# Kernel tuning notes

Measured on AMD Instinct MI355X. Metric: run time of the kernel, lower is better.

The kernel has to match this reference:

```python
import jax, jax.numpy as jnp
import numpy as np
from jax import lax

# Model hyperparameters (match init_kwargs)
DIM = 512
N_HEADS = 8
HEAD_DIM = DIM // N_HEADS
N_LAYERS = 4
N_LEVELS = 3          # len(chunk_sizes); CMS forward = stack of MLPs per level
HIDDEN = 4 * DIM
VOCAB = 50257
MAX_SEQ = 2048
B, S = 1, 2048
LN_EPS = 1e-5


def layer_norm(x, w, b):
    m = x.mean(-1, keepdims=True)
    v = ((x - m) ** 2).mean(-1, keepdims=True)
    return (x - m) * lax.rsqrt(v + LN_EPS) * w + b


def linear_attention(x, wq, wk, wv, wo):
    """LinearAttentionWithMemory: fast-weight recurrence M += k v^T, ksum += k,
    y_t = (M_t q_t) / (ksum_t . q_t + 1e-6). x: (B,S,DIM). Weights stored (in,out)."""
    Bn, Sn, D = x.shape
    fmap = lambda z: jax.nn.elu(z) + 1.0  # elu(x)+1 feature map
    # (B,S,D) -> (S,B,H,d) for scan over time
    def proj(w):
        return fmap(x @ w).reshape(Bn, Sn, N_HEADS, HEAD_DIM).transpose(1, 0, 2, 3)
    q = proj(wq)
    k = proj(wk)
    v = fmap(x @ wv).reshape(Bn, Sn, N_HEADS, HEAD_DIM).transpose(1, 0, 2, 3)
    # NOTE: original applies feature_map only to Q and K; V is raw projection
    v = (x @ wv).reshape(Bn, Sn, N_HEADS, HEAD_DIM).transpose(1, 0, 2, 3)

    def step(carry, inp):
        M, ksum = carry            # M: (B,H,d,d), ksum: (B,H,d)
        q_t, k_t, v_t = inp        # each (B,H,d)
        M = M + k_t[..., :, None] * v_t[..., None, :]
        ksum = ksum + k_t
        num = jnp.einsum('bhde,bhd->bhe', M, q_t)
        den = jnp.einsum('bhd,bhd->bh', ksum, q_t)[..., None] + 1e-6
        return (M, ksum), num / den

    carry0 = (jnp.zeros((Bn, N_HEADS, HEAD_DIM, HEAD_DIM), x.dtype),
              jnp.zeros((Bn, N_HEADS, HEAD_DIM), x.dtype))
    _, ys = lax.scan(step, carry0, (q, k, v))          # ys: (S,B,H,d)
    out = ys.transpose(1, 0, 2, 3).reshape(Bn, Sn, D)
    return out @ wo


def cms(x, w1, b1, w2, b2):
    """Continuum Memory System forward: sequential chain of per-level MLPs
    (chunk sizes only control parameter-update frequency during training).
    w1: (N_LEVELS, DIM, HIDDEN), w2: (N_LEVELS, HIDDEN, DIM)."""
    h = x
    for lvl in range(N_LEVELS):
        h = jax.nn.gelu(h @ w1[lvl] + b1[lvl]) @ w2[lvl] + b2[lvl]
    return h


def setup_inputs() -> dict:
    key = jax.random.key(0)
    ks = jax.random.split(key, 16)
    std = 0.02
    inp = {
        'tok_emb': jax.random.normal(ks[0], (VOCAB, DIM), jnp.float32) * std,
        'pos_emb': jax.random.normal(ks[1], (MAX_SEQ, DIM), jnp.float32) * std,
        'ln1_w': jnp.ones((N_LAYERS, DIM), jnp.float32),
        'ln1_b': jnp.zeros((N_LAYERS, DIM), jnp.float32),
        'wq': jax.random.normal(ks[2], (N_LAYERS, DIM, DIM), jnp.float32) * std,
        'wk': jax.random.normal(ks[3], (N_LAYERS, DIM, DIM), jnp.float32) * std,
        'wv': jax.random.normal(ks[4], (N_LAYERS, DIM, DIM), jnp.float32) * std,
        'wo': jax.random.normal(ks[5], (N_LAYERS, DIM, DIM), jnp.float32) * std,
        'ln2_w': jnp.ones((N_LAYERS, DIM), jnp.float32),
        'ln2_b': jnp.zeros((N_LAYERS, DIM), jnp.float32),
        'cms_w1': jax.random.normal(ks[6], (N_LAYERS, N_LEVELS, DIM, HIDDEN), jnp.float32) * std,
        'cms_b1': jnp.zeros((N_LAYERS, N_LEVELS, HIDDEN), jnp.float32),
        'cms_w2': jax.random.normal(ks[7], (N_LAYERS, N_LEVELS, HIDDEN, DIM), jnp.float32) * std,
        'cms_b2': jnp.zeros((N_LAYERS, N_LEVELS, DIM), jnp.float32),
        'lnf_w': jnp.ones((DIM,), jnp.float32),
        'lnf_b': jnp.zeros((DIM,), jnp.float32),
        'input_ids': jax.random.randint(ks[8], (B, S), 0, VOCAB, jnp.int32),
    }
    return inp


def reference(tok_emb, pos_emb, ln1_w, ln1_b, wq, wk, wv, wo,
              ln2_w, ln2_b, cms_w1, cms_b1, cms_w2, cms_b2,
              lnf_w, lnf_b, input_ids):
    seq_len = input_ids.shape[1]
    x = tok_emb[input_ids] + pos_emb[:seq_len][None, :, :]
    for l in range(N_LAYERS):
        x = x + linear_attention(layer_norm(x, ln1_w[l], ln1_b[l]),
                                 wq[l], wk[l], wv[l], wo[l])
        x = x + cms(layer_norm(x, ln2_w[l], ln2_b[l]),
                    cms_w1[l], cms_b1[l], cms_w2[l], cms_b2[l])
    x = layer_norm(x, lnf_w, lnf_b)
    logits = x @ tok_emb.T  # tied head weights
    return logits
```

## Files before the change

kernel.cpp:

```cpp
#include <hip/hip_runtime.h>

#define SQL 2048
#define DIM 512
#define NHEADS 8
#define HD 64
#define NLAYERS 4
#define NLEVELS 3
#define HID 2048
#define VOC 50257
#define CHUNK 64
#define NCHUNK 32
#define SD (SQL * DIM)
#define DD (DIM * DIM)

typedef __attribute__((ext_vector_type(8))) short bf16x8;
typedef __attribute__((ext_vector_type(4))) float f32x4;

__device__ __forceinline__ float gelu_f(float x) {
    float x3 = x * x * x;
    return 0.5f * x * (1.f + tanhf(0.7978845608028654f * (x + 0.044715f * x3)));
}
__device__ __forceinline__ float fmap_f(float x) {
    return x > 0.f ? x + 1.f : expf(x);
}
__device__ __forceinline__ unsigned short f2bf(float x) {
    unsigned int u = __float_as_uint(x);
    u = (u + 0x7fffu + ((u >> 16) & 1u)) >> 16;
    return (unsigned short)u;
}
__device__ __forceinline__ float bf2f(unsigned short h) {
    return __uint_as_float(((unsigned int)h) << 16);
}

__global__ __launch_bounds__(256) void embed_k(
    const float* __restrict__ tok, const float* __restrict__ pos,
    const int* __restrict__ ids, float* __restrict__ x)
{
    int idx = blockIdx.x * 256 + threadIdx.x;
    int t = idx >> 9;
    int d = idx & 511;
    x[idx] = tok[(size_t)ids[t] * DIM + d] + pos[idx];
}

__global__ __launch_bounds__(256) void ln_k(
    const float* __restrict__ in, unsigned short* __restrict__ oh,
    unsigned short* __restrict__ ol,
    const float* __restrict__ w, const float* __restrict__ b)
{
    int t = blockIdx.x, tid = threadIdx.x;
    float v0 = in[t * DIM + tid];
    float v1 = in[t * DIM + 256 + tid];
    float s = v0 + v1, sq = v0 * v0 + v1 * v1;
    #pragma unroll
    for (int off = 32; off > 0; off >>= 1) {
        s  += __shfl_down(s, off);
        sq += __shfl_down(sq, off);
    }
    __shared__ float ss[4], sqs[4];
    int wave = tid >> 6, lane = tid & 63;
    if (lane == 0) { ss[wave] = s; sqs[wave] = sq; }
    __syncthreads();
    float S  = ss[0] + ss[1] + ss[2] + ss[3];
    float SQ = sqs[0] + sqs[1] + sqs[2] + sqs[3];
    float m   = S * (1.f / DIM);
    float var = SQ * (1.f / DIM) - m * m;
    float rs  = rsqrtf(var + 1e-5f);
    float y0 = (v0 - m) * rs * w[tid]       + b[tid];
    float y1 = (v1 - m) * rs * w[256 + tid] + b[256 + tid];
    unsigned short h0 = f2bf(y0), h1 = f2bf(y1);
    oh[t * DIM + tid]       = h0;
    ol[t * DIM + tid]       = f2bf(y0 - bf2f(h0));
    oh[t * DIM + 256 + tid] = h1;
    ol[t * DIM + 256 + tid] = f2bf(y1 - bf2f(h1));
}

__global__ __launch_bounds__(256) void conv_rh_k(
    const float* __restrict__ in, unsigned short* __restrict__ oh, long long n4)
{
    long long i = (long long)blockIdx.x * 256 + threadIdx.x;
    if (i >= n4) return;
    float4 v = ((const float4*)in)[i];
    ushort4 hh;
    hh.x = f2bf(v.x); hh.y = f2bf(v.y); hh.z = f2bf(v.z); hh.w = f2bf(v.w);
    ((ushort4*)oh)[i] = hh;
}

__global__ __launch_bounds__(256) void conv_t_k(
    const float* __restrict__ in, unsigned short* __restrict__ oh,
    unsigned short* __restrict__ ol, int K, int N,
    size_t srcZ, size_t dstZ)
{
    in += (size_t)blockIdx.z * srcZ;
    oh += (size_t)blockIdx.z * dstZ;
    ol += (size_t)blockIdx.z * dstZ;
    __shared__ float T[32][33];
    const int n0 = blockIdx.x * 32, k0 = blockIdx.y * 32;
    const int tr = threadIdx.x >> 3, tc = threadIdx.x & 7;
    float4 v = *(const float4*)(in + (size_t)(k0 + tr) * N + n0 + tc * 4);
    T[tr][tc * 4 + 0] = v.x;
    T[tr][tc * 4 + 1] = v.y;
    T[tr][tc * 4 + 2] = v.z;
    T[tr][tc * 4 + 3] = v.w;
    __syncthreads();
    float o0 = T[tc * 4 + 0][tr];
    float o1 = T[tc * 4 + 1][tr];
    float o2 = T[tc * 4 + 2][tr];
    float o3 = T[tc * 4 + 3][tr];
    unsigned short h0 = f2bf(o0), h1 = f2bf(o1), h2 = f2bf(o2), h3 = f2bf(o3);
    ushort4 hh; hh.x = h0; hh.y = h1; hh.z = h2; hh.w = h3;
    ushort4 ll;
    ll.x = f2bf(o0 - bf2f(h0));
    ll.y = f2bf(o1 - bf2f(h1));
    ll.z = f2bf(o2 - bf2f(h2));
    ll.w = f2bf(o3 - bf2f(h3));
    size_t off = (size_t)(n0 + tr) * K + k0 + tc * 4;
    *(ushort4*)(oh + off) = hh;
    *(ushort4*)(ol + off) = ll;
}

template<int ACT, bool RES, bool PLANES, bool NG, bool X3, bool MSWAP, int BN>
__global__ __launch_bounds__(256) void gemm_t(
    const unsigned short* __restrict__ Ah, const unsigned short* __restrict__ Al,
    const unsigned short* __restrict__ Bh, const unsigned short* __restrict__ Bl,
    const float* __restrict__ bias, const float* __restrict__ Rsrc,
    float* __restrict__ C, unsigned short* __restrict__ Oh,
    unsigned short* __restrict__ Ol,
    int M, int N, int K, int fthr)
{
    constexpr int NW = BN / 2;
    constexpr int NF = NW / 16;
    __shared__ unsigned short sAh[4096], sAl[4096];
    __shared__ unsigned short sBh[BN * 32];
    __shared__ unsigned short sBl[X3 ? BN * 32 : 64];

    const int tid  = threadIdx.x;
    const int w    = tid >> 6, lane = tid & 63;
    const int r    = lane & 15, kq = lane >> 4;
    const int wr   = w >> 1, wc = w & 1;
    const int m0   = (MSWAP ? blockIdx.x : blockIdx.y) * 128;
    const int n0   = (MSWAP ? blockIdx.y : blockIdx.x) * BN;

    const int srow = tid >> 2;
    const int sch  = tid & 3;
    const int ar0 = m0 + srow, ar1 = ar0 + 64;
    int br0 = n0 + srow;
    if (NG) br0 = br0 < N ? br0 : N - 1;
    const unsigned short* pAh0 = Ah + (size_t)ar0 * K + sch * 8;
    const unsigned short* pAh1 = Ah + (size_t)ar1 * K + sch * 8;
    const unsigned short* pAl0 = Al + (size_t)ar0 * K + sch * 8;
    const unsigned short* pAl1 = Al + (size_t)ar1 * K + sch * 8;
    const unsigned short* pBh0 = Bh + (size_t)br0 * K + sch * 8;
    const unsigned short* pBl0 = X3 ? Bl + (size_t)br0 * K + sch * 8 : nullptr;
    const unsigned short* pBh1 = nullptr;
    const unsigned short* pBl1 = nullptr;
    if constexpr (BN == 128) {
        int br1 = n0 + 64 + srow;
        if (NG) br1 = br1 < N ? br1 : N - 1;
        pBh1 = Bh + (size_t)br1 * K + sch * 8;
        if constexpr (X3) pBl1 = Bl + (size_t)br1 * K + sch * 8;
    }

    bf16x8 rAh0 = *(const bf16x8*)pAh0, rAh1 = *(const bf16x8*)pAh1;
    bf16x8 rAl0 = *(const bf16x8*)pAl0, rAl1 = *(const bf16x8*)pAl1;
    bf16x8 rBh0 = *(const bf16x8*)pBh0;
    bf16x8 rBh1{}, rBl0{}, rBl1{};
    if constexpr (X3) rBl0 = *(const bf16x8*)pBl0;
    if constexpr (BN == 128) {
        rBh1 = *(const bf16x8*)pBh1;
        if constexpr (X3) rBl1 = *(const bf16x8*)pBl1;
    }

    f32x4 acc[4][NF] = {};
    const int sw = tid * 8;

    for (int ks = 0; ks < K; ks += 32) {
        __syncthreads();
        *(bf16x8*)&sAh[sw] = rAh0;  *(bf16x8*)&sAh[sw + 2048] = rAh1;
        *(bf16x8*)&sAl[sw] = rAl0;  *(bf16x8*)&sAl[sw + 2048] = rAl1;
        *(bf16x8*)&sBh[sw] = rBh0;
        if constexpr (BN == 128) *(bf16x8*)&sBh[sw + 2048] = rBh1;
        if constexpr (X3) {
            *(bf16x8*)&sBl[sw] = rBl0;
            if constexpr (BN == 128) *(bf16x8*)&sBl[sw + 2048] = rBl1;
        }
        __syncthreads();

        if (ks + 32 < K) {
            pAh0 += 32; pAh1 += 32; pAl0 += 32; pAl1 += 32;
            pBh0 += 32;
            rAh0 = *(const bf16x8*)pAh0; rAh1 = *(const bf16x8*)pAh1;
            rAl0 = *(const bf16x8*)pAl0; rAl1 = *(const bf16x8*)pAl1;
            rBh0 = *(const bf16x8*)pBh0;
            if constexpr (X3) { pBl0 += 32; rBl0 = *(const bf16x8*)pBl0; }
            if constexpr (BN == 128) {
                pBh1 += 32; rBh1 = *(const bf16x8*)pBh1;
                if constexpr (X3) { pBl1 += 32; rBl1 = *(const bf16x8*)pBl1; }
            }
        }

        bf16x8 a_h[4], a_l[4];
        #pragma unroll
        for (int mi = 0; mi < 4; ++mi) {
            const int off = (wr * 64 + mi * 16 + r) * 32 + kq * 8;
            a_h[mi] = *(const bf16x8*)&sAh[off];
            a_l[mi] = *(const bf16x8*)&sAl[off];
        }
        #pragma unroll
        for (int ni = 0; ni < NF; ++ni) {
            const int off = (wc * NW + ni * 16 + r) * 32 + kq * 8;
            const bf16x8 b_h = *(const bf16x8*)&sBh[off];
            #pragma unroll
            for (int mi = 0; mi < 4; ++mi) {
                acc[mi][ni] = __builtin_amdgcn_mfma_f32_16x16x32_bf16(
                    a_h[mi], b_h, acc[mi][ni], 0, 0, 0);
                acc[mi][ni] = __builtin_amdgcn_mfma_f32_16x16x32_bf16(
                    a_l[mi], b_h, acc[mi][ni], 0, 0, 0);
            }
            if constexpr (X3) {
                const bf16x8 b_l = *(const bf16x8*)&sBl[off];
                #pragma unroll
                for (int mi = 0; mi < 4; ++mi)
                    acc[mi][ni] = __builtin_amdgcn_mfma_f32_16x16x32_bf16(
                        a_h[mi], b_l, acc[mi][ni], 0, 0, 0);
            }
        }
    }

    #pragma unroll
    for (int mi = 0; mi < 4; ++mi)
        #pragma unroll
        for (int ni = 0; ni < NF; ++ni) {
            const int nn = n0 + wc * NW + ni * 16 + r;
            if (NG && nn >= N) continue;
            #pragma unroll
            for (int g = 0; g < 4; ++g) {
                const int mm = m0 + wr * 64 + mi * 16 + kq * 4 + g;
                float v = acc[mi][ni][g];
                if (bias) v += bias[nn];
                if (ACT == 2) v = gelu_f(v);
                if (ACT == 3) v = (nn < fthr) ? fmap_f(v) : v;
                const size_t o = (size_t)mm * N + nn;
                if (PLANES) {
                    unsigned short h = f2bf(v);
                    Oh[o] = h;
                    Ol[o] = f2bf(v - bf2f(h));
                } else {
                    if (RES) v += Rsrc[o];
                    C[o] = v;
                }
            }
        }
}

template<int ACT, bool RES, bool PLANES>
__global__ __launch_bounds__(256) void gemm_ks(
    const unsigned short* __restrict__ Ah, const unsigned short* __restrict__ Al,
    const unsigned short* __restrict__ Bh, const unsigned short* __restrict__ Bl,
    const float* __restrict__ bias, const float* __restrict__ Rsrc,
    float* __restrict__ C, unsigned short* __restrict__ Oh,
    unsigned short* __restrict__ Ol,
    int M, int N, int K, int fthr)
{
    const int tid  = threadIdx.x;
    const int w    = tid >> 6;
    const int lane = tid & 63;
    const int r  = lane & 15;
    const int kq = lane >> 4;
    const int m0 = blockIdx.y * 64, n0 = blockIdx.x * 64;
    const int Kw = K >> 2;

    f32x4 acc[4][4] = {};

    size_t aoff[4], boff[4];
    #pragma unroll
    for (int i = 0; i < 4; ++i) {
        aoff[i] = (size_t)(m0 + i * 16 + r) * K + w * Kw + kq * 8;
        boff[i] = (size_t)(n0 + i * 16 + r) * K + w * Kw + kq * 8;
    }

    for (int k0 = 0; k0 < Kw; k0 += 32) {
        bf16x8 ah[4], al4[4], bh[4], bl4[4];
        #pragma unroll
        for (int i = 0; i < 4; ++i) {
            ah[i]  = *(const bf16x8*)(Ah + aoff[i] + k0);
            al4[i] = *(const bf16x8*)(Al + aoff[i] + k0);
            bh[i]  = *(const bf16x8*)(Bh + boff[i] + k0);
            bl4[i] = *(const bf16x8*)(Bl + boff[i] + k0);
        }
        #pragma unroll
        for (int mi = 0; mi < 4; ++mi)
            #pragma unroll
            for (int ni = 0; ni < 4; ++ni) {
                acc[mi][ni] = __builtin_amdgcn_mfma_f32_16x16x32_bf16(
                    ah[mi], bh[ni], acc[mi][ni], 0, 0, 0);
                acc[mi][ni] = __builtin_amdgcn_mfma_f32_16x16x32_bf16(
                    ah[mi], bl4[ni], acc[mi][ni], 0, 0, 0);
                acc[mi][ni] = __builtin_amdgcn_mfma_f32_16x16x32_bf16(
                    al4[mi], bh[ni], acc[mi][ni], 0, 0, 0);
            }
    }

    __shared__ f32x4 red[4][64][8];

    #pragma unroll
    for (int R = 0; R < 2; ++R) {
        if (R) __syncthreads();
        #pragma unroll
        for (int mh = 0; mh < 2; ++mh) {
            const int mi = R * 2 + mh;
            const int q2 = mh * 4 + kq;
            #pragma unroll
            for (int ni = 0; ni < 4; ++ni) {
                const int cc = ni * 16 + r;
                red[w][cc][q2 ^ (cc & 7)] = acc[mi][ni];
            }
        }
        __syncthreads();
        const int col = lane;
        #pragma unroll
        for (int g = 0; g < 2; ++g) {
            const int q2 = w * 2 + g;
            const int swz = q2 ^ (col & 7);
            f32x4 s = red[0][col][swz];
            s += red[1][col][swz];
            s += red[2][col][swz];
            s += red[3][col][swz];
            const int gn = n0 + col;
            float bv = bias ? bias[gn] : 0.f;
            #pragma unroll
            for (int e = 0; e < 4; ++e) {
                const int gm = m0 + R * 32 + q2 * 4 + e;
                float v = s[e] + bv;
                if (ACT == 2) v = gelu_f(v);
                if (ACT == 3) v = (gn < fthr) ? fmap_f(v) : v;
                const size_t o = (size_t)gm * N + gn;
                if (PLANES) {
                    unsigned short h = f2bf(v);
                    Oh[o] = h;
                    Ol[o] = f2bf(v - bf2f(h));
                } else {
                    if (RES) v += Rsrc[o];
                    C[o] = v;
                }
            }
        }
    }
}

__global__ __launch_bounds__(256) void attn_p1(
    const float* __restrict__ kbuf, const float* __restrict__ vbuf,
    float* __restrict__ Mc, float* __restrict__ ksum, int rs)
{
    const int h = blockIdx.x >> 5, c = blockIdx.x & 31;
    const int tid = threadIdx.x;
    const int tx = tid & 15, ty = tid >> 4;
    __shared__ float Ks[CHUNK][HD + 1];
    __shared__ float Vs[CHUNK][HD + 1];
    #pragma unroll
    for (int i = 0; i < 16; ++i) {
        int idx = tid + i * 256;
        int t = idx >> 6, d = idx & 63;
        size_t g = (size_t)(c * CHUNK + t) * rs + h * HD + d;
        Ks[t][d] = kbuf[g];
        Vs[t][d] = vbuf[g];
    }
    __syncthreads();

    float acc[4][4] = {};
    for (int t = 0; t < CHUNK; ++t) {
        float ka[4], vb[4];
        #pragma unroll
        for (int i = 0; i < 4; ++i) ka[i] = Ks[t][ty * 4 + i];
        #pragma unroll
        for (int j = 0; j < 4; ++j) vb[j] = Vs[t][tx * 4 + j];
        #pragma unroll
        for (int i = 0; i < 4; ++i)
            #pragma unroll
            for (int j = 0; j < 4; ++j)
                acc[i][j] += ka[i] * vb[j];
    }
    const size_t base = (size_t)(h * NCHUNK + c) * HD * HD;
    #pragma unroll
    for (int i = 0; i < 4; ++i)
        #pragma unroll
        for (int j = 0; j < 4; ++j)
            Mc[base + (size_t)(ty * 4 + i) * HD + tx * 4 + j] = acc[i][j];

    if (tid < HD) {
        float s = 0.f;
        for (int t = 0; t < CHUNK; ++t) s += Ks[t][tid];
        ksum[(size_t)(h * NCHUNK + c) * HD + tid] = s;
    }
}

__global__ __launch_bounds__(64) void attn_scan(
    float* __restrict__ Mc, float* __restrict__ ksum)
{
    const int b = blockIdx.x;
    const int h = b / 65, p = b % 65;
    const int tid = threadIdx.x;
    float v[NCHUNK];
    if (p < HD) {
        const size_t base = ((size_t)(h * NCHUNK) * HD + p) * HD + tid;
        #pragma unroll
        for (int c = 0; c < NCHUNK; ++c)
            v[c] = Mc[base + (size_t)c * HD * HD];
        float run = 0.f;
        #pragma unroll
        for (int c = 0; c < NCHUNK; ++c) {
            Mc[base + (size_t)c * HD * HD] = run;
            run += v[c];
        }
    } else {
        const size_t base = (size_t)(h * NCHUNK) * HD + tid;
        #pragma unroll
        for (int c = 0; c < NCHUNK; ++c)
            v[c] = ksum[base + (size_t)c * HD];
        float run = 0.f;
        #pragma unroll
        for (int c = 0; c < NCHUNK; ++c) {
            ksum[base + (size_t)c * HD] = run;
            run += v[c];
        }
    }
}

__global__ __launch_bounds__(256) void attn_p3(
    const float* __restrict__ qbuf, const float* __restrict__ kbuf,
    const float* __restrict__ vbuf, const float* __restrict__ Mc,
    const float* __restrict__ ksum,
    unsigned short* __restrict__ aoh, unsigned short* __restrict__ aol, int rs)
{
    const int h = blockIdx.x >> 5, c = blockIdx.x & 31;
    const int tid = threadIdx.x;
    const int tx = tid & 15, ty = tid >> 4;
    __shared__ float Qs[CHUNK][HD + 1];
    __shared__ float Ks[CHUNK][HD + 1];
    __shared__ float Vs[CHUNK][HD + 1];
    __shared__ float Ss[CHUNK][CHUNK + 1];
    __shared__ float Ms[HD][HD + 1];
    __shared__ float kp[HD], den[CHUNK];

    const size_t mbase = (size_t)(h * NCHUNK + c) * HD * HD;
    #pragma unroll
    for (int i = 0; i < 16; ++i) {
        int idx = tid + i * 256;
        int t = idx >> 6, d = idx & 63;
        size_t g = (size_t)(c * CHUNK + t) * rs + h * HD + d;
        Qs[t][d] = qbuf[g];
        Ks[t][d] = kbuf[g];
        Vs[t][d] = vbuf[g];
        Ms[t][d] = Mc[mbase + (size_t)t * HD + d];
    }
    if (tid < HD) kp[tid] = ksum[(size_t)(h * NCHUNK + c) * HD + tid];
    __syncthreads();

    {
        float acc[4][4] = {};
        for (int d = 0; d < HD; ++d) {
            float qa[4], kb[4];
            #pragma unroll
            for (int i = 0; i < 4; ++i) qa[i] = Qs[ty * 4 + i][d];
            #pragma unroll
            for (int j = 0; j < 4; ++j) kb[j] = Ks[tx * 4 + j][d];
            #pragma unroll
            for (int i = 0; i < 4; ++i)
                #pragma unroll
                for (int j = 0; j < 4; ++j)
                    acc[i][j] += qa[i] * kb[j];
        }
        #pragma unroll
        for (int i = 0; i < 4; ++i)
            #pragma unroll
            for (int j = 0; j < 4; ++j) {
                int t = ty * 4 + i, u = tx * 4 + j;
                Ss[t][u] = (u <= t) ? acc[i][j] : 0.f;
            }
    }
    __syncthreads();

    if (tid < CHUNK) {
        int t = tid;
        float s = 1e-6f;
        for (int d = 0; d < HD; ++d) s += Qs[t][d] * kp[d];
        for (int u = 0; u < CHUNK; ++u) s += Ss[t][u];
        den[t] = s;
    }
    __syncthreads();

    {
        float acc[4][4] = {};
        for (int d = 0; d < HD; ++d) {
            float qa[4], mb[4];
            #pragma unroll
            for (int i = 0; i < 4; ++i) qa[i] = Qs[ty * 4 + i][d];
            #pragma unroll
            for (int j = 0; j < 4; ++j) mb[j] = Ms[d][tx * 4 + j];
            #pragma unroll
            for (int i = 0; i < 4; ++i)
                #pragma unroll
                for (int j = 0; j < 4; ++j)
                    acc[i][j] += qa[i] * mb[j];
        }
        for (int u = 0; u < CHUNK; ++u) {
            float sa[4], vb[4];
            #pragma unroll
            for (int i = 0; i < 4; ++i) sa[i] = Ss[ty * 4 + i][u];
            #pragma unroll
            for (int j = 0; j < 4; ++j) vb[j] = Vs[u][tx * 4 + j];
            #pragma unroll
            for (int i = 0; i < 4; ++i)
                #pragma unroll
                for (int j = 0; j < 4; ++j)
                    acc[i][j] += sa[i] * vb[j];
        }
        #pragma unroll
        for (int i = 0; i < 4; ++i) {
            int t = ty * 4 + i;
            float inv = 1.f / den[t];
            #pragma unroll
            for (int j = 0; j < 4; ++j) {
                float vv = acc[i][j] * inv;
                unsigned short hh = f2bf(vv);
                size_t o = (size_t)(c * CHUNK + t) * DIM + h * HD + tx * 4 + j;
                aoh[o] = hh;
                aol[o] = f2bf(vv - bf2f(hh));
            }
        }
    }
}

extern "C" void kernel_launch(void* const* d_in, const int* in_sizes, int n_in,
                              void* d_out, int out_size, void* d_ws, size_t ws_size,
                              hipStream_t stream)
{
    const float* tok  = (const float*)d_in[0];
    const float* pos  = (const float*)d_in[1];
    const float* ln1w = (const float*)d_in[2];
    const float* ln1b = (const float*)d_in[3];
    const float* wq   = (const float*)d_in[4];
    const float* wk   = (const float*)d_in[5];
    const float* wv   = (const float*)d_in[6];
    const float* wo   = (const float*)d_in[7];
    const float* ln2w = (const float*)d_in[8];
    const float* ln2b = (const float*)d_in[9];
    const float* w1   = (const float*)d_in[10];
    const float* b1   = (const float*)d_in[11];
    const float* w2   = (const float*)d_in[12];
    const float* b2   = (const float*)d_in[13];
    const float* lnfw = (const float*)d_in[14];
    const float* lnfb = (const float*)d_in[15];
    const int*   ids  = (const int*)d_in[16];
    float* outp = (float*)d_out;

    typedef unsigned short us;
    char* p = (char*)d_ws;
    float* x   = (float*)p; p += (size_t)SD * 4;
    float* qkv = (float*)p; p += (size_t)SQL * 3 * DIM * 4;
    float* Mc  = (float*)p; p += (size_t)NHEADS * NCHUNK * HD * HD * 4;
    float* ksm = (float*)p; p += (size_t)NHEADS * NCHUNK * HD * 4;

    us* xnH = (us*)p; p += (size_t)SD * 2;
    us* xnL = (us*)p; p += (size_t)SD * 2;
    us* aoH = (us*)p; p += (size_t)SD * 2;
    us* aoL = (us*)p; p += (size_t)SD * 2;
    us* cinH = (us*)p; p += (size_t)SD * 2;
    us* cinL = (us*)p; p += (size_t)SD * 2;
    us* h1H = (us*)p; p += (size_t)SQL * HID * 2;
    us* h1L = (us*)p; p += (size_t)SQL * HID * 2;
    us* tokH = (us*)p; p += (size_t)VOC * DIM * 2;
    us* wqkvH = (us*)p; p += (size_t)NLAYERS * 3 * DD * 2;
    us* wqkvL = (us*)p; p += (size_t)NLAYERS * 3 * DD * 2;
    us* woH = (us*)p; p += (size_t)NLAYERS * DD * 2;
    us* woL = (us*)p; p += (size_t)NLAYERS * DD * 2;
    const size_t W1SZ = (size_t)NLAYERS * NLEVELS * DIM * HID;
    us* w1H = (us*)p; p += W1SZ * 2;
    us* w1L = (us*)p; p += W1SZ * 2;
    us* w2H = (us*)p; p += W1SZ * 2;
    us* w2L = (us*)p; p += W1SZ * 2;

    {
        long long n4 = (long long)VOC * DIM / 4;
        conv_rh_k<<<(unsigned)((n4 + 255) / 256), 256, 0, stream>>>(tok, tokH, n4);
        dim3 gt(DIM / 32, DIM / 32, NLAYERS);
        conv_t_k<<<gt, 256, 0, stream>>>(wq, wqkvH,          wqkvL,          DIM, DIM, DD, (size_t)3 * DD);
        conv_t_k<<<gt, 256, 0, stream>>>(wk, wqkvH + DD,     wqkvL + DD,     DIM, DIM, DD, (size_t)3 * DD);
        conv_t_k<<<gt, 256, 0, stream>>>(wv, wqkvH + 2 * DD, wqkvL + 2 * DD, DIM, DIM, DD, (size_t)3 * DD);
        conv_t_k<<<gt, 256, 0, stream>>>(wo, woH, woL, DIM, DIM, DD, DD);
        dim3 g1(HID / 32, DIM / 32, NLAYERS * NLEVELS);
        conv_t_k<<<g1, 256, 0, stream>>>(w1, w1H, w1L, DIM, HID,
                                         (size_t)DIM * HID, (size_t)DIM * HID);
        dim3 g2(DIM / 32, HID / 32, NLAYERS * NLEVELS);
        conv_t_k<<<g2, 256, 0, stream>>>(w2, w2H, w2L, HID, DIM,
                                         (size_t)DIM * HID, (size_t)DIM * HID);
    }

    embed_k<<<SD / 256, 256, 0, stream>>>(tok, pos, ids, x);

    const dim3 gqkv(3 * DIM / 64, SQL / 128);
    const dim3 g512(DIM / 64, SQL / 64);
    const dim3 gw1(HID / 64, SQL / 128);
    const dim3 ghead(SQL / 128, (VOC + 127) / 128);
    const int RS = 3 * DIM;

    for (int l = 0; l < NLAYERS; ++l) {
        ln_k<<<SQL, 256, 0, stream>>>(x, xnH, xnL, ln1w + l * DIM, ln1b + l * DIM);
        gemm_t<3, false, false, false, true, false, 64><<<gqkv, 256, 0, stream>>>(
            xnH, xnL, wqkvH + (size_t)l * 3 * DD, wqkvL + (size_t)l * 3 * DD,
            nullptr, nullptr, qkv, nullptr, nullptr, SQL, 3 * DIM, DIM, 2 * DIM);
        attn_p1<<<NHEADS * NCHUNK, 256, 0, stream>>>(qkv + DIM, qkv + 2 * DIM, Mc, ksm, RS);
        attn_scan<<<NHEADS * 65, 64, 0, stream>>>(Mc, ksm);
        attn_p3<<<NHEADS * NCHUNK, 256, 0, stream>>>(
            qkv, qkv + DIM, qkv + 2 * DIM, Mc, ksm, aoH, aoL, RS);
        gemm_ks<0, true, false><<<g512, 256, 0, stream>>>(
            aoH, aoL, woH + (size_t)l * DD, woL + (size_t)l * DD,
            nullptr, x, x, nullptr, nullptr, SQL, DIM, DIM, 0);

        ln_k<<<SQL, 256, 0, stream>>>(x, xnH, xnL, ln2w + l * DIM, ln2b + l * DIM);
        const us* cH = xnH; const us* cL = xnL;
        for (int lvl = 0; lvl < NLEVELS; ++lvl) {
            const size_t off1 = (size_t)(l * NLEVELS + lvl) * DIM * HID;
            const float* b1p = b1 + (size_t)(l * NLEVELS + lvl) * HID;
            const float* b2p = b2 + (size_t)(l * NLEVELS + lvl) * DIM;
            gemm_t<2, false, true, false, true, false, 64><<<gw1, 256, 0, stream>>>(
                cH, cL, w1H + off1, w1L + off1, b1p, nullptr,
                nullptr, h1H, h1L, SQL, HID, DIM, 0);
            if (lvl < NLEVELS - 1) {
                gemm_ks<0, false, true><<<g512, 256, 0, stream>>>(
                    h1H, h1L, w2H + off1, w2L + off1, b2p, nullptr,
                    nullptr, cinH, cinL, SQL, DIM, HID, 0);
                cH = cinH; cL = cinL;
            } else {
                gemm_ks<0, true, false><<<g512, 256, 0, stream>>>(
                    h1H, h1L, w2H + off1, w2L + off1, b2p, x,
                    x, nullptr, nullptr, SQL, DIM, HID, 0);
            }
        }
    }

    ln_k<<<SQL, 256, 0, stream>>>(x, xnH, xnL, lnfw, lnfb);
    gemm_t<0, false, false, true, false, true, 128><<<ghead, 256, 0, stream>>>(
        xnH, xnL, tokH, nullptr, nullptr, nullptr,
        outp, nullptr, nullptr, SQL, VOC, DIM, 0);
}
```

Before: 1.873 ms.

## Double-buffer GEMM LDS tiles using direct global-to-LDS async loads

Replaces register-staged global loads plus LDS stores in the split-bf16 GEMM with global_load_lds builtins that write straight into LDS. LDS tiles are now double-buffered so the next K-slice loads while the current one feeds MFMAs, with one barrier per iteration instead of two. This aims to hide global memory latency and cut register pressure. In exchange it doubles LDS use, which may lower occupancy, and it relies on the per-wave LDS offset layout matching the old thread-to-slot mapping. Correctness also depends on the barrier ordering the async LDS writes before they are read.

```diff
diff --git a/kernel.cpp b/kernel.cpp
--- a/kernel.cpp
+++ b/kernel.cpp
@@ -30,6 +30,12 @@
 }
 __device__ __forceinline__ float bf2f(unsigned short h) {
     return __uint_as_float(((unsigned int)h) << 16);
+}
+
+__device__ __forceinline__ void gl16(const void* g, void* l) {
+    __builtin_amdgcn_global_load_lds(
+        (const __attribute__((address_space(1))) void*)g,
+        (__attribute__((address_space(3))) void*)l, 16, 0, 0);
 }
 
 __global__ __launch_bounds__(256) void embed_k(
@@ -129,9 +135,9 @@
 {
     constexpr int NW = BN / 2;
     constexpr int NF = NW / 16;
-    __shared__ unsigned short sAh[4096], sAl[4096];
-    __shared__ unsigned short sBh[BN * 32];
-    __shared__ unsigned short sBl[X3 ? BN * 32 : 64];
+    __shared__ unsigned short sAh[2][4096], sAl[2][4096];
+    __shared__ unsigned short sBh[2][BN * 32];
+    __shared__ unsigned short sBl[X3 ? 2 : 1][X3 ? BN * 32 : 64];
 
     const int tid  = threadIdx.x;
     const int w    = tid >> 6, lane = tid & 63;
@@ -139,6 +145,7 @@
     const int wr   = w >> 1, wc = w & 1;
     const int m0   = (MSWAP ? blockIdx.x : blockIdx.y) * 128;
     const int n0   = (MSWAP ? blockIdx.y : blockIdx.x) * BN;
+    const int wofs = w * 1024;
 
     const int srow = tid >> 2;
     const int sch  = tid & 3;
@@ -160,55 +167,49 @@
         if constexpr (X3) pBl1 = Bl + (size_t)br1 * K + sch * 8;
     }
 
-    bf16x8 rAh0 = *(const bf16x8*)pAh0, rAh1 = *(const bf16x8*)pAh1;
-    bf16x8 rAl0 = *(const bf16x8*)pAl0, rAl1 = *(const bf16x8*)pAl1;
-    bf16x8 rBh0 = *(const bf16x8*)pBh0;
-    bf16x8 rBh1{}, rBl0{}, rBl1{};
-    if constexpr (X3) rBl0 = *(const bf16x8*)pBl0;
-    if constexpr (BN == 128) {
-        rBh1 = *(const bf16x8*)pBh1;
-        if constexpr (X3) rBl1 = *(const bf16x8*)pBl1;
-    }
+    auto stage = [&](int bb) {
+        char* aH = (char*)&sAh[bb][0] + wofs;
+        char* aL = (char*)&sAl[bb][0] + wofs;
+        char* bH = (char*)&sBh[bb][0] + wofs;
+        gl16(pAh0, aH);        gl16(pAh1, aH + 4096);
+        gl16(pAl0, aL);        gl16(pAl1, aL + 4096);
+        gl16(pBh0, bH);
+        if constexpr (BN == 128) gl16(pBh1, bH + 4096);
+        if constexpr (X3) {
+            char* bL = (char*)&sBl[bb][0] + wofs;
+            gl16(pBl0, bL);
+            if constexpr (BN == 128) gl16(pBl1, bL + 4096);
+        }
+    };
 
     f32x4 acc[4][NF] = {};
-    const int sw = tid * 8;
-
+
+    stage(0);
+    __syncthreads();
+    int bb = 0;
     for (int ks = 0; ks < K; ks += 32) {
-        __syncthreads();
-        *(bf16x8*)&sAh[sw] = rAh0;  *(bf16x8*)&sAh[sw + 2048] = rAh1;
-        *(bf16x8*)&sAl[sw] = rAl0;  *(bf16x8*)&sAl[sw + 2048] = rAl1;
-        *(bf16x8*)&sBh[sw] = rBh0;
-        if constexpr (BN == 128) *(bf16x8*)&sBh[sw + 2048] = rBh1;
-        if constexpr (X3) {
-            *(bf16x8*)&sBl[sw] = rBl0;
-            if constexpr (BN == 128) *(bf16x8*)&sBl[sw + 2048] = rBl1;
-        }
-        __syncthreads();
-
         if (ks + 32 < K) {
             pAh0 += 32; pAh1 += 32; pAl0 += 32; pAl1 += 32;
             pBh0 += 32;
-            rAh0 = *(const bf16x8*)pAh0; rAh1 = *(const bf16x8*)pAh1;
-            rAl0 = *(const bf16x8*)pAl0; rAl1 = *(const bf16x8*)pAl1;
-            rBh0 = *(const bf16x8*)pBh0;
-            if constexpr (X3) { pBl0 += 32; rBl0 = *(const bf16x8*)pBl0; }
-            if constexpr (BN == 128) {
-                pBh1 += 32; rBh1 = *(const bf16x8*)pBh1;
-                if constexpr (X3) { pBl1 += 32; rBl1 = *(const bf16x8*)pBl1; }
-            }
+            if constexpr (BN == 128) pBh1 += 32;
+            if constexpr (X3) {
+                pBl0 += 32;
+                if constexpr (BN == 128) pBl1 += 32;
+            }
+            stage(bb ^ 1);
         }
 
         bf16x8 a_h[4], a_l[4];
         #pragma unroll
         for (int mi = 0; mi < 4; ++mi) {
             const int off = (wr * 64 + mi * 16 + r) * 32 + kq * 8;
-            a_h[mi] = *(const bf16x8*)&sAh[off];
-            a_l[mi] = *(const bf16x8*)&sAl[off];
+            a_h[mi] = *(const bf16x8*)&sAh[bb][off];
+            a_l[mi] = *(const bf16x8*)&sAl[bb][off];
         }
         #pragma unroll
         for (int ni = 0; ni < NF; ++ni) {
             const int off = (wc * NW + ni * 16 + r) * 32 + kq * 8;
-            const bf16x8 b_h = *(const bf16x8*)&sBh[off];
+            const bf16x8 b_h = *(const bf16x8*)&sBh[bb][off];
             #pragma unroll
             for (int mi = 0; mi < 4; ++mi) {
                 acc[mi][ni] = __builtin_amdgcn_mfma_f32_16x16x32_bf16(
@@ -217,13 +218,15 @@
                     a_l[mi], b_h, acc[mi][ni], 0, 0, 0);
             }
             if constexpr (X3) {
-                const bf16x8 b_l = *(const bf16x8*)&sBl[off];
+                const bf16x8 b_l = *(const bf16x8*)&sBl[bb][off];
                 #pragma unroll
                 for (int mi = 0; mi < 4; ++mi)
                     acc[mi][ni] = __builtin_amdgcn_mfma_f32_16x16x32_bf16(
                         a_h[mi], b_l, acc[mi][ni], 0, 0, 0);
             }
         }
+        __syncthreads();
+        bb ^= 1;
     }
 
     #pragma unroll
```

Result: slower. 1.912 ms (+2.1%).
